# Kernel tuning notes

Measured on AMD Instinct MI355X. Metric: run time of the kernel, lower is better.

## Reference

```python
import jax, jax.numpy as jnp
import numpy as np

N_NODES, N_EDGES, N_FEAT, EMB, N_GRAPHS = 500_000, 16_000_000, 16, 4, 1024


def setup_inputs() -> dict:
    key = jax.random.key(0)
    ks = jax.random.split(key, 12)
    x = jax.random.normal(ks[0], (N_NODES, N_FEAT), jnp.float32)
    edge_index = jax.random.randint(ks[1], (2, N_EDGES), 0, N_NODES, dtype=jnp.int32)
    batch_index = jnp.sort(jax.random.randint(ks[2], (N_NODES,), 0, N_GRAPHS, dtype=jnp.int32))
    s = 1.0 / np.sqrt(N_FEAT)
    W0 = jax.random.uniform(ks[3], (N_FEAT, EMB), jnp.float32, -s, s)
    b0 = jnp.zeros((EMB,), jnp.float32)
    se = 1.0 / np.sqrt(EMB)
    Wc = jax.random.uniform(ks[4], (6, EMB, EMB), jnp.float32, -se, se)  # conv1..conv6
    bc = jnp.zeros((6, EMB), jnp.float32)
    H = EMB * 14  # 56 pooled features
    sh = 1.0 / np.sqrt(H)
    Wout = jax.random.uniform(ks[5], (H, H), jnp.float32, -sh, sh)
    bout = jax.random.uniform(ks[6], (H,), jnp.float32, -sh, sh)
    Wout2 = jax.random.uniform(ks[7], (H, 1), jnp.float32, -sh, sh)
    bout2 = jax.random.uniform(ks[8], (1,), jnp.float32, -sh, sh)
    return {"x": x, "edge_index": edge_index, "batch_index": batch_index,
            "num_graphs": N_GRAPHS, "W0": W0, "b0": b0, "Wc": Wc, "bc": bc,
            "Wout": Wout, "bout": bout, "Wout2": Wout2, "bout2": bout2}


def reference(x, edge_index, batch_index, num_graphs, W0, b0, Wc, bc, Wout, bout, Wout2, bout2):
    N = x.shape[0]
    src, dst = edge_index[0], edge_index[1]
    loop = jnp.arange(N, dtype=src.dtype)
    src_f = jnp.concatenate([src, loop])  # add self-loops (PyG GCNConv default)
    dst_f = jnp.concatenate([dst, loop])
    deg = jax.ops.segment_sum(jnp.ones_like(dst_f, dtype=x.dtype), dst_f, num_segments=N)
    dis = jnp.where(deg > 0, jax.lax.rsqrt(deg), 0.0)
    norm = dis[src_f] * dis[dst_f]  # [E+N]

    def conv(h, W, b):
        xw = h @ W  # linear first, as in PyG GCNConv
        agg = jax.ops.segment_sum(norm[:, None] * xw[src_f], dst_f, num_segments=N)
        return agg + b

    hs = [conv(x, W0, b0)]
    for i in range(6):
        hs.append(conv(hs[-1], Wc[i], bc[i]))

    counts = jnp.maximum(
        jax.ops.segment_sum(jnp.ones((N,), x.dtype), batch_index, num_segments=num_graphs), 1.0)
    pooled = []
    for h in hs:
        pooled.append(jax.ops.segment_max(h, batch_index, num_segments=num_graphs))
        pooled.append(jax.ops.segment_sum(h, batch_index, num_segments=num_graphs) / counts[:, None])
    hcat = jnp.concatenate(pooled, axis=1)  # [G, 56]
    z = jax.nn.relu(hcat @ Wout + bout)
    logit = z @ Wout2 + bout2  # [G, 1]
    return jax.nn.sigmoid(logit), logit
```

## Files before the change

kernel.cpp:

```cpp
#include <hip/hip_runtime.h>
#include <hip/hip_fp16.h>
#include <math.h>

#define TPB 256
#define HB 512
#define BSH 10
#define TILE 32768
#define SRCBITS 19
#define SRCMASK ((1u << SRCBITS) - 1)
#define CAP 17408

__device__ inline unsigned pk2(float a, float b) {
    union { __half2 h2; unsigned u; } cv;
    cv.h2 = __halves2half2(__float2half_rn(a), __float2half_rn(b));
    return cv.u;
}
__device__ inline float2 upk2(unsigned u) {
    union { unsigned u; __half2 h2; } cv; cv.u = u;
    return __half22float2(cv.h2);
}
__device__ inline unsigned encf(float x) {
    unsigned u = __float_as_uint(x);
    return (u & 0x80000000u) ? ~u : (u | 0x80000000u);
}
__device__ inline float decf(unsigned e) {
    unsigned u = (e & 0x80000000u) ? (e & 0x7FFFFFFFu) : ~e;
    return __uint_as_float(u);
}


__global__ void histA_kernel(const int* __restrict__ dst, int* __restrict__ tileHist, int E) {
    __shared__ int h[HB];
    int t = threadIdx.x;
    for (int i = t; i < HB; i += TPB) h[i] = 0;
    __syncthreads();
    int base = blockIdx.x * TILE;
#pragma unroll
    for (int k = 0; k < TILE / (TPB * 4); k++) {
        int e = base + (k * TPB + t) * 4;
        if (e < E) {
            int4 d = *(const int4*)(dst + e);
            atomicAdd(&h[((unsigned)d.x) >> BSH], 1);
            atomicAdd(&h[((unsigned)d.y) >> BSH], 1);
            atomicAdd(&h[((unsigned)d.z) >> BSH], 1);
            atomicAdd(&h[((unsigned)d.w) >> BSH], 1);
        }
    }
    __syncthreads();
    int* out = tileHist + (size_t)blockIdx.x * HB;
    for (int i = t; i < HB; i += TPB) out[i] = h[i];
}

__global__ void btot_kernel(const int* __restrict__ tileHist, int* __restrict__ totals, int nTiles) {
    __shared__ int sh[TPB];
    int b = blockIdx.x, t = threadIdx.x;
    int s = 0;
    for (int i = t; i < nTiles; i += TPB) s += tileHist[(size_t)i * HB + b];
    sh[t] = s; __syncthreads();
    for (int d = TPB / 2; d > 0; d >>= 1) { if (t < d) sh[t] += sh[t + d]; __syncthreads(); }
    if (t == 0) totals[b] = sh[0];
}

__global__ void bscan_kernel(const int* __restrict__ totals, int* __restrict__ bucketStart) {
    __shared__ int sh[TPB];
    int t = threadIdx.x;
    int v0 = totals[t * 2], v1 = totals[t * 2 + 1];
    int s = v0 + v1;
    sh[t] = s; __syncthreads();
    for (int d = 1; d < TPB; d <<= 1) {
        int x = (t >= d) ? sh[t - d] : 0; __syncthreads();
        sh[t] += x; __syncthreads();
    }
    int excl = sh[t] - s;
    bucketStart[t * 2] = excl;
    bucketStart[t * 2 + 1] = excl + v0;
    if (t == TPB - 1) bucketStart[HB] = sh[TPB - 1];
}

__global__ void tbase_kernel(const int* __restrict__ tileHist, const int* __restrict__ bucketStart,
                             int* __restrict__ tileBase, int nTiles) {
    __shared__ int sh[TPB];
    int b = blockIdx.x, t = threadIdx.x;
    const int CH = 8;
    int pre[CH]; int s = 0;
#pragma unroll
    for (int k = 0; k < CH; k++) {
        int i = t * CH + k;
        int v = (i < nTiles) ? tileHist[(size_t)i * HB + b] : 0;
        pre[k] = s; s += v;
    }
    sh[t] = s; __syncthreads();
    for (int d = 1; d < TPB; d <<= 1) {
        int x = (t >= d) ? sh[t - d] : 0; __syncthreads();
        sh[t] += x; __syncthreads();
    }
    int excl = sh[t] - s;
    int bs = bucketStart[b];
#pragma unroll
    for (int k = 0; k < CH; k++) {
        int i = t * CH + k;
        if (i < nTiles) tileBase[(size_t)i * HB + b] = bs + excl + pre[k];
    }
}

__global__ void scatterC_kernel(const int* __restrict__ src, const int* __restrict__ dst,
                                const int* __restrict__ tileBase, unsigned* __restrict__ bucketed, int E) {
    __shared__ int cur[HB];
    int t = threadIdx.x;
    const int* tb = tileBase + (size_t)blockIdx.x * HB;
    for (int i = t; i < HB; i += TPB) cur[i] = tb[i];
    __syncthreads();
    int base = blockIdx.x * TILE;
#pragma unroll
    for (int k = 0; k < TILE / (TPB * 4); k++) {
        int e = base + (k * TPB + t) * 4;
        if (e < E) {
            int4 s4 = *(const int4*)(src + e);
            int4 d4 = *(const int4*)(dst + e);
            {
                int b = ((unsigned)d4.x) >> BSH;
                int pos = atomicAdd(&cur[b], 1);
                bucketed[pos] = ((unsigned)s4.x) | ((((unsigned)d4.x) & ((1u << BSH) - 1)) << SRCBITS);
            }
            {
                int b = ((unsigned)d4.y) >> BSH;
                int pos = atomicAdd(&cur[b], 1);
                bucketed[pos] = ((unsigned)s4.y) | ((((unsigned)d4.y) & ((1u << BSH) - 1)) << SRCBITS);
            }
            {
                int b = ((unsigned)d4.z) >> BSH;
                int pos = atomicAdd(&cur[b], 1);
                bucketed[pos] = ((unsigned)s4.z) | ((((unsigned)d4.z) & ((1u << BSH) - 1)) << SRCBITS);
            }
            {
                int b = ((unsigned)d4.w) >> BSH;
                int pos = atomicAdd(&cur[b], 1);
                bucketed[pos] = ((unsigned)s4.w) | ((((unsigned)d4.w) & ((1u << BSH) - 1)) << SRCBITS);
            }
        }
    }
}

__global__ __launch_bounds__(TPB) void buildD_kernel(
        const unsigned* __restrict__ bucketed, const int* __restrict__ bucketStart,
        int* __restrict__ csr, int* __restrict__ off, float* __restrict__ dis,
        int N, int E, int nbuk) {
    const int DR = 512;
    __shared__ int h[DR];
    __shared__ int loc[DR];
    __shared__ int sh[TPB];
    __shared__ int totLow;
    __shared__ int stage[CAP];
    int blk = blockIdx.x;
    int b = blk >> 1, half = blk & 1;
    int t = threadIdx.x;
    int p0 = bucketStart[b], p1 = bucketStart[b + 1];
    for (int i = t; i < DR; i += TPB) h[i] = 0;
    if (t == 0) totLow = 0;
    __syncthreads();

    int aBeg = (p0 + 3) & ~3; if (aBeg > p1) aBeg = p1;
    int aEnd = p1 & ~3;        if (aEnd < aBeg) aEnd = aBeg;
    int lowCnt = 0;
    for (int p = p0 + t; p < aBeg; p += TPB) {
        int j = (int)(bucketed[p] >> SRCBITS);
        if ((j >> 9) == half) atomicAdd(&h[j & 511], 1);
        else if (half) lowCnt++;
    }
    for (int p = aBeg + t * 4; p < aEnd; p += TPB * 4) {
        uint4 v4 = *(const uint4*)(bucketed + p);
        unsigned vv[4] = {v4.x, v4.y, v4.z, v4.w};
#pragma unroll
        for (int q = 0; q < 4; q++) {
            int j = (int)(vv[q] >> SRCBITS);
            if ((j >> 9) == half) atomicAdd(&h[j & 511], 1);
            else if (half) lowCnt++;
        }
    }
    for (int p = aEnd + t; p < p1; p += TPB) {
        int j = (int)(bucketed[p] >> SRCBITS);
        if ((j >> 9) == half) atomicAdd(&h[j & 511], 1);
        else if (half) lowCnt++;
    }
    if (half && lowCnt) atomicAdd(&totLow, lowCnt);
    __syncthreads();

    int v0 = h[t * 2], v1 = h[t * 2 + 1];
    int s = v0 + v1;
    sh[t] = s; __syncthreads();
    for (int d = 1; d < TPB; d <<= 1) {
        int x = (t >= d) ? sh[t - d] : 0; __syncthreads();
        sh[t] += x; __syncthreads();
    }
    int excl = sh[t] - s;
    int base = p0 + (half ? totLow : 0);
    int dstBase = (b << BSH) + (half << 9);
    {
        int j0 = t * 2, j1 = j0 + 1;
        loc[j0] = excl;
        loc[j1] = excl + v0;
        int d0 = dstBase + j0, d1 = dstBase + j1;
        if (d0 < N) { off[d0] = base + excl;      dis[d0] = rsqrtf((float)(v0 + 1)); }
        if (d1 < N) { off[d1] = base + excl + v0; dis[d1] = rsqrtf((float)(v1 + 1)); }
    }
    if (b == nbuk - 1 && half == 1 && t == 0) off[N] = E;
    int cnt = sh[TPB - 1];
    __syncthreads();

    for (int p = p0 + t; p < aBeg; p += TPB) {
        unsigned v = bucketed[p];
        int j = (int)(v >> SRCBITS);
        if ((j >> 9) == half) {
            int pos = atomicAdd(&loc[j & 511], 1);
            int sv = (int)(v & SRCMASK);
            if (pos < CAP) stage[pos] = sv; else csr[base + pos] = sv;
        }
    }
    for (int p = aBeg + t * 4; p < aEnd; p += TPB * 4) {
        uint4 v4 = *(const uint4*)(bucketed + p);
        unsigned vv[4] = {v4.x, v4.y, v4.z, v4.w};
#pragma unroll
        for (int q = 0; q < 4; q++) {
            int j = (int)(vv[q] >> SRCBITS);
            if ((j >> 9) == half) {
                int pos = atomicAdd(&loc[j & 511], 1);
                int sv = (int)(vv[q] & SRCMASK);
                if (pos < CAP) stage[pos] = sv; else csr[base + pos] = sv;
            }
        }
    }
    for (int p = aEnd + t; p < p1; p += TPB) {
        unsigned v = bucketed[p];
        int j = (int)(v >> SRCBITS);
        if ((j >> 9) == half) {
            int pos = atomicAdd(&loc[j & 511], 1);
            int sv = (int)(v & SRCMASK);
            if (pos < CAP) stage[pos] = sv; else csr[base + pos] = sv;
        }
    }
    __syncthreads();
    int c = cnt < CAP ? cnt : CAP;
    for (int i = t; i < c; i += TPB) csr[base + i] = stage[i];
}


__global__ void g0_kernel(const float* __restrict__ x, const float* __restrict__ W0,
                          const float* __restrict__ dis, uint2* __restrict__ g, int N) {
    __shared__ float W[64];
    int t = threadIdx.x;
    if (t < 64) W[t] = W0[t];
    __syncthreads();
    int v = blockIdx.x * blockDim.x + t;
    if (v >= N) return;
    const float4* xp = (const float4*)(x + (size_t)v * 16);
    float o0 = 0.f, o1 = 0.f, o2 = 0.f, o3 = 0.f;
#pragma unroll
    for (int q = 0; q < 4; q++) {
        float4 xv = xp[q];
        float xk[4] = {xv.x, xv.y, xv.z, xv.w};
#pragma unroll
        for (int r = 0; r < 4; r++) {
            int k = q * 4 + r;
            o0 += xk[r] * W[k * 4 + 0];
            o1 += xk[r] * W[k * 4 + 1];
            o2 += xk[r] * W[k * 4 + 2];
            o3 += xk[r] * W[k * 4 + 3];
        }
    }
    float dv = dis[v];
    g[v] = make_uint2(pk2(dv * o0, dv * o1), pk2(dv * o2, dv * o3));
}

__global__ void agg_kernel(const int* __restrict__ off, const int* __restrict__ csr,
                           const uint2* __restrict__ gin, const float* __restrict__ dis,
                           const int* __restrict__ batch,
                           const float* __restrict__ bias, const float* __restrict__ Wn,
                           uint2* __restrict__ gout,
                           unsigned* __restrict__ pmax, float* __restrict__ psum,
                           int L, int N) {
    __shared__ float hx[64], hy[64], hz[64], hw[64];
    __shared__ int gid[64];
    int t = threadIdx.x;
    int lane = t & 3;
    int slot = t >> 2;
    int v = blockIdx.x * 64 + slot;
    bool valid = v < N;
    float sx = 0.f, sy = 0.f, sz = 0.f, sw = 0.f;
    float tx = 0.f, ty = 0.f, tz = 0.f, tw = 0.f;
    if (valid) {
        int p0 = off[v], p1 = off[v + 1];
        if (lane == 0) {
            uint2 r = gin[v];
            float2 a = upk2(r.x), b = upk2(r.y);
            sx = a.x; sy = a.y; sz = b.x; sw = b.y;
        }
        int p = p0 + lane;
        for (; p + 4 < p1; p += 8) {
            int i0 = csr[p], i1 = csr[p + 4];
            uint2 r0 = gin[i0];
            uint2 r1 = gin[i1];
            float2 a0 = upk2(r0.x), b0 = upk2(r0.y);
            float2 a1 = upk2(r1.x), b1 = upk2(r1.y);
            sx += a0.x; sy += a0.y; sz += b0.x; sw += b0.y;
            tx += a1.x; ty += a1.y; tz += b1.x; tw += b1.y;
        }
        if (p < p1) {
            uint2 r = gin[csr[p]];
            float2 a = upk2(r.x), b = upk2(r.y);
            sx += a.x; sy += a.y; sz += b.x; sw += b.y;
        }
        sx += tx; sy += ty; sz += tz; sw += tw;
    }
    sx += __shfl_xor(sx, 1); sy += __shfl_xor(sy, 1); sz += __shfl_xor(sz, 1); sw += __shfl_xor(sw, 1);
    sx += __shfl_xor(sx, 2); sy += __shfl_xor(sy, 2); sz += __shfl_xor(sz, 2); sw += __shfl_xor(sw, 2);
    if (lane == 0) {
        if (valid) {
            float dv = dis[v];
            float h0 = dv * sx + bias[0];
            float h1 = dv * sy + bias[1];
            float h2 = dv * sz + bias[2];
            float h3 = dv * sw + bias[3];
            hx[slot] = h0; hy[slot] = h1; hz[slot] = h2; hw[slot] = h3;
            gid[slot] = batch[v];
            if (Wn) {
                float o0 = h0 * Wn[0] + h1 * Wn[4] + h2 * Wn[8]  + h3 * Wn[12];
                float o1 = h0 * Wn[1] + h1 * Wn[5] + h2 * Wn[9]  + h3 * Wn[13];
                float o2 = h0 * Wn[2] + h1 * Wn[6] + h2 * Wn[10] + h3 * Wn[14];
                float o3 = h0 * Wn[3] + h1 * Wn[7] + h2 * Wn[11] + h3 * Wn[15];
                gout[v] = make_uint2(pk2(dv * o0, dv * o1), pk2(dv * o2, dv * o3));
            }
        } else {
            gid[slot] = -1;
        }
    }
    __syncthreads();
    if (t < 64) {
        int g = gid[t];
        if (g >= 0 && (t == 0 || gid[t - 1] != g)) {
            float m0 = -INFINITY, m1 = -INFINITY, m2 = -INFINITY, m3 = -INFINITY;
            float s0 = 0.f, s1 = 0.f, s2 = 0.f, s3 = 0.f;
            for (int i = t; i < 64 && gid[i] == g; i++) {
                m0 = fmaxf(m0, hx[i]); s0 += hx[i];
                m1 = fmaxf(m1, hy[i]); s1 += hy[i];
                m2 = fmaxf(m2, hz[i]); s2 += hz[i];
                m3 = fmaxf(m3, hw[i]); s3 += hw[i];
            }
            unsigned* pm = pmax + (size_t)g * 28 + L * 4;
            float*    ps = psum + (size_t)g * 28 + L * 4;
            atomicMax(&pm[0], encf(m0)); atomicMax(&pm[1], encf(m1));
            atomicMax(&pm[2], encf(m2)); atomicMax(&pm[3], encf(m3));
            atomicAdd(&ps[0], s0); atomicAdd(&ps[1], s1);
            atomicAdd(&ps[2], s2); atomicAdd(&ps[3], s3);
        }
    }
}


__global__ void bounds_kernel(const int* __restrict__ batch, int* __restrict__ start,
                              int N, int ng) {
    int g = blockIdx.x * blockDim.x + threadIdx.x;
    if (g > ng) return;
    if (g == ng) { start[ng] = N; return; }
    int lo = 0, hi = N;
    while (lo < hi) {
        int mid = (lo + hi) >> 1;
        if (batch[mid] < g) lo = mid + 1; else hi = mid;
    }
    start[g] = lo;
}


__global__ void mlp_kernel(const unsigned* __restrict__ pmax, const float* __restrict__ psum,
                           const int* __restrict__ start,
                           const float* __restrict__ Wout, const float* __restrict__ bout,
                           const float* __restrict__ Wout2, const float* __restrict__ bout2,
                           float* __restrict__ out, int ng) {
    __shared__ float hc[56];
    __shared__ float zz[56];
    int gph = blockIdx.x;
    int t = threadIdx.x;
    if (t < 56) {
        int L = t >> 3, k = t & 7;
        size_t base = (size_t)gph * 28 + L * 4;
        float val;
        if (k < 4) {
            val = decf(pmax[base + k]);
        } else {
            int cnt = start[gph + 1] - start[gph];
            float inv = 1.0f / (float)(cnt > 0 ? cnt : 1);
            val = psum[base + (k - 4)] * inv;
        }
        hc[t] = val;
    }
    __syncthreads();
    if (t < 56) {
        float acc = bout[t];
        for (int k = 0; k < 56; k++) acc += hc[k] * Wout[k * 56 + t];
        zz[t] = fmaxf(acc, 0.f);
    }
    __syncthreads();
    float val = (t < 56) ? zz[t] * Wout2[t] : 0.f;
#pragma unroll
    for (int d = 32; d > 0; d >>= 1) val += __shfl_down(val, d, 64);
    if (t == 0) {
        float logit = val + bout2[0];
        out[gph] = 1.f / (1.f + expf(-logit));
        out[ng + gph] = logit;
    }
}


extern "C" void kernel_launch(void* const* d_in, const int* in_sizes, int n_in,
                              void* d_out, int out_size, void* d_ws, size_t ws_size,
                              hipStream_t stream) {
    const float* x     = (const float*)d_in[0];
    const int*   ei    = (const int*)d_in[1];
    const int*   batch = (const int*)d_in[2];
    const float* W0    = (const float*)d_in[4];
    const float* b0    = (const float*)d_in[5];
    const float* Wc    = (const float*)d_in[6];
    const float* bc    = (const float*)d_in[7];
    const float* Wout  = (const float*)d_in[8];
    const float* bout  = (const float*)d_in[9];
    const float* Wout2 = (const float*)d_in[10];
    const float* bout2 = (const float*)d_in[11];

    const int N  = in_sizes[0] / 16;
    const int E  = in_sizes[1] / 2;
    const int ng = 1024;
    const int* srcp = ei;
    const int* dstp = ei + E;
    const int nTiles = (E + TILE - 1) / TILE;
    const int nbuk   = (N + (1 << BSH) - 1) >> BSH;

    char* w = (char*)d_ws;
    auto alloc = [&](size_t bytes) -> char* {
        char* p = w;
        w += (bytes + 255) & ~(size_t)255;
        return p;
    };
    int*      csr         = (int*)alloc((size_t)E * 4);
    unsigned* bucketed    = (unsigned*)alloc((size_t)E * 4);
    int*      tileHist    = (int*)alloc((size_t)nTiles * HB * 4);
    int*      tileBase    = (int*)alloc((size_t)nTiles * HB * 4);
    int*      totals      = (int*)alloc((size_t)HB * 4);
    int*      bucketStart = (int*)alloc((size_t)(HB + 1) * 4);
    int*      off         = (int*)alloc((size_t)(N + 1) * 4);
    float*    dis         = (float*)alloc((size_t)N * 4);
    int*      start       = (int*)alloc((size_t)(ng + 1) * 4);
    unsigned* pmax        = (unsigned*)alloc((size_t)ng * 28 * 4);
    float*    psum        = (float*)alloc((size_t)ng * 28 * 4);
    uint2*    gA = (uint2*)bucketed;
    uint2*    gB = gA + N;

    histA_kernel<<<nTiles, TPB, 0, stream>>>(dstp, tileHist, E);
    btot_kernel<<<HB, TPB, 0, stream>>>(tileHist, totals, nTiles);
    bscan_kernel<<<1, TPB, 0, stream>>>(totals, bucketStart);
    tbase_kernel<<<HB, TPB, 0, stream>>>(tileHist, bucketStart, tileBase, nTiles);
    scatterC_kernel<<<nTiles, TPB, 0, stream>>>(srcp, dstp, tileBase, bucketed, E);
    buildD_kernel<<<nbuk * 2, TPB, 0, stream>>>(bucketed, bucketStart, csr, off, dis, N, E, nbuk);
    bounds_kernel<<<(ng + 1 + TPB - 1) / TPB, TPB, 0, stream>>>(batch, start, N, ng);
    hipMemsetAsync(pmax, 0, (size_t)ng * 28 * 4, stream);
    hipMemsetAsync(psum, 0, (size_t)ng * 28 * 4, stream);

    const int gbN = (N + TPB - 1) / TPB;
    g0_kernel<<<gbN, TPB, 0, stream>>>(x, W0, dis, gA, N);

    const int gbAgg = (N + 63) / 64;
    uint2* gin = gA;
    uint2* gout = gB;
    for (int L = 0; L < 7; ++L) {
        const float* bias = (L == 0) ? b0 : bc + (size_t)(L - 1) * 4;
        const float* Wn   = (L < 6) ? Wc + (size_t)L * 16 : nullptr;
        agg_kernel<<<gbAgg, TPB, 0, stream>>>(off, csr, gin, dis, batch, bias, Wn,
                                              gout, pmax, psum, L, N);
        uint2* tmp = gin; gin = gout; gout = tmp;
    }

    mlp_kernel<<<ng, 64, 0, stream>>>(pmax, psum, start, Wout, bout, Wout2, bout2,
                                      (float*)d_out, ng);
}
```

Baseline: 1.365 ms.

## Stage edge scatter in shared memory for coalesced bucket writes; nontemporal CSR loads

The edge-bucketing scatter kernel now builds a per-tile histogram, sorts the tile's packed edges into shared memory by bucket, and then writes each bucket's run to global memory contiguously with one wave per bucket. Before, every edge was written straight to a scattered global position. The tile size is halved so the 64 KB staging buffer fits in LDS. This adds a second read of dst and extra LDS traffic, and it lowers occupancy. Separately, CSR index loads in the aggregation kernel become nontemporal so they do not evict the gathered feature rows from cache.

```diff
diff --git a/kernel.cpp b/kernel.cpp
--- a/kernel.cpp
+++ b/kernel.cpp
@@ -5,7 +5,7 @@
 #define TPB 256
 #define HB 512
 #define BSH 10
-#define TILE 32768
+#define TILE 16384
 #define SRCBITS 19
 #define SRCMASK ((1u << SRCBITS) - 1)
 #define CAP 17408
@@ -103,41 +103,69 @@
     }
 }
 
-__global__ void scatterC_kernel(const int* __restrict__ src, const int* __restrict__ dst,
-                                const int* __restrict__ tileBase, unsigned* __restrict__ bucketed, int E) {
-    __shared__ int cur[HB];
-    int t = threadIdx.x;
-    const int* tb = tileBase + (size_t)blockIdx.x * HB;
-    for (int i = t; i < HB; i += TPB) cur[i] = tb[i];
+__global__ __launch_bounds__(TPB) void scatterC_kernel(
+        const int* __restrict__ src, const int* __restrict__ dst,
+        const int* __restrict__ tileBase, unsigned* __restrict__ bucketed, int E) {
+    __shared__ int h[HB];
+    __shared__ int hstart[HB];
+    __shared__ int loc[HB];
+    __shared__ int sh[TPB];
+    __shared__ unsigned stage[TILE];
+    int t = threadIdx.x;
+    for (int i = t; i < HB; i += TPB) h[i] = 0;
     __syncthreads();
     int base = blockIdx.x * TILE;
+#pragma unroll
+    for (int k = 0; k < TILE / (TPB * 4); k++) {
+        int e = base + (k * TPB + t) * 4;
+        if (e < E) {
+            int4 d4 = *(const int4*)(dst + e);
+            atomicAdd(&h[((unsigned)d4.x) >> BSH], 1);
+            atomicAdd(&h[((unsigned)d4.y) >> BSH], 1);
+            atomicAdd(&h[((unsigned)d4.z) >> BSH], 1);
+            atomicAdd(&h[((unsigned)d4.w) >> BSH], 1);
+        }
+    }
+    __syncthreads();
+    int v0 = h[t * 2], v1 = h[t * 2 + 1];
+    int s = v0 + v1;
+    sh[t] = s; __syncthreads();
+    for (int d = 1; d < TPB; d <<= 1) {
+        int x = (t >= d) ? sh[t - d] : 0; __syncthreads();
+        sh[t] += x; __syncthreads();
+    }
+    int excl = sh[t] - s;
+    hstart[t * 2] = excl;         loc[t * 2] = excl;
+    hstart[t * 2 + 1] = excl + v0; loc[t * 2 + 1] = excl + v0;
+    __syncthreads();
 #pragma unroll
     for (int k = 0; k < TILE / (TPB * 4); k++) {
         int e = base + (k * TPB + t) * 4;
         if (e < E) {
             int4 s4 = *(const int4*)(src + e);
             int4 d4 = *(const int4*)(dst + e);
-            {
-                int b = ((unsigned)d4.x) >> BSH;
-                int pos = atomicAdd(&cur[b], 1);
-                bucketed[pos] = ((unsigned)s4.x) | ((((unsigned)d4.x) & ((1u << BSH) - 1)) << SRCBITS);
-            }
-            {
-                int b = ((unsigned)d4.y) >> BSH;
-                int pos = atomicAdd(&cur[b], 1);
-                bucketed[pos] = ((unsigned)s4.y) | ((((unsigned)d4.y) & ((1u << BSH) - 1)) << SRCBITS);
-            }
-            {
-                int b = ((unsigned)d4.z) >> BSH;
-                int pos = atomicAdd(&cur[b], 1);
-                bucketed[pos] = ((unsigned)s4.z) | ((((unsigned)d4.z) & ((1u << BSH) - 1)) << SRCBITS);
-            }
-            {
-                int b = ((unsigned)d4.w) >> BSH;
-                int pos = atomicAdd(&cur[b], 1);
-                bucketed[pos] = ((unsigned)s4.w) | ((((unsigned)d4.w) & ((1u << BSH) - 1)) << SRCBITS);
-            }
-        }
+            int b0 = ((unsigned)d4.x) >> BSH;
+            int p0 = atomicAdd(&loc[b0], 1);
+            stage[p0] = ((unsigned)s4.x) | ((((unsigned)d4.x) & ((1u << BSH) - 1)) << SRCBITS);
+            int b1 = ((unsigned)d4.y) >> BSH;
+            int p1 = atomicAdd(&loc[b1], 1);
+            stage[p1] = ((unsigned)s4.y) | ((((unsigned)d4.y) & ((1u << BSH) - 1)) << SRCBITS);
+            int b2 = ((unsigned)d4.z) >> BSH;
+            int p2 = atomicAdd(&loc[b2], 1);
+            stage[p2] = ((unsigned)s4.z) | ((((unsigned)d4.z) & ((1u << BSH) - 1)) << SRCBITS);
+            int b3 = ((unsigned)d4.w) >> BSH;
+            int p3 = atomicAdd(&loc[b3], 1);
+            stage[p3] = ((unsigned)s4.w) | ((((unsigned)d4.w) & ((1u << BSH) - 1)) << SRCBITS);
+        }
+    }
+    __syncthreads();
+    const int* tb = tileBase + (size_t)blockIdx.x * HB;
+    int wave = t >> 6, lane = t & 63;
+    for (int b = wave; b < HB; b += 4) {
+        int sb = hstart[b], eb = loc[b];
+        int gb = tb[b];
+        for (int i = sb + lane; i < eb; i += 64)
+            bucketed[gb + (i - sb)] = stage[i];
     }
 }
 
@@ -296,7 +324,8 @@
         }
         int p = p0 + lane;
         for (; p + 4 < p1; p += 8) {
-            int i0 = csr[p], i1 = csr[p + 4];
+            int i0 = __builtin_nontemporal_load(csr + p);
+            int i1 = __builtin_nontemporal_load(csr + p + 4);
             uint2 r0 = gin[i0];
             uint2 r1 = gin[i1];
             float2 a0 = upk2(r0.x), b0 = upk2(r0.y);
@@ -305,7 +334,8 @@
             tx += a1.x; ty += a1.y; tz += b1.x; tw += b1.y;
         }
         if (p < p1) {
-            uint2 r = gin[csr[p]];
+            int i0 = __builtin_nontemporal_load(csr + p);
+            uint2 r = gin[i0];
             float2 a = upk2(r.x), b = upk2(r.y);
             sx += a.x; sy += a.y; sz += b.x; sw += b.y;
         }
```

After: 1.481 ms. 8.5% more time.
